# Kernel tuning notes

Measured on AMD Instinct MI355X. Metric: run time of the kernel, lower is better.

Reference implementation:

```python
import jax, jax.numpy as jnp
import numpy as np

DIM = 128
NH = 4
K = 7
PAD = K // 2  # dilation = 1
MLP_HID = 4 * DIM
EPS = 1e-5


def _layernorm(x, w, b):
    m = jnp.mean(x, axis=-1, keepdims=True)
    v = jnp.mean((x - m) ** 2, axis=-1, keepdims=True)
    return (x - m) / jnp.sqrt(v + EPS) * w + b


def _windows(xp, H, W):
    # xp: [B, nh, Hp, Wp, hd] zero-padded; returns [B, nh, H, W, hd, K*K]
    return jnp.stack(
        [xp[:, :, i:i + H, j:j + W, :] for i in range(K) for j in range(K)],
        axis=-1,
    )


def setup_inputs() -> dict:
    key = jax.random.key(0)
    ks = jax.random.split(key, 10)
    s = 0.02
    inp = {
        "x": jax.random.normal(ks[0], (4, 56, 56, DIM), dtype=jnp.float32),
        "ln1_w": jnp.ones((DIM,), jnp.float32),
        "ln1_b": jnp.zeros((DIM,), jnp.float32),
        "w_qkv": jax.random.normal(ks[1], (DIM, 3 * DIM), jnp.float32) * s,
        "b_qkv": jnp.zeros((3 * DIM,), jnp.float32),
        "rpb": jax.random.normal(ks[2], (NH, K * K), jnp.float32) * s,
        "w_proj": jax.random.normal(ks[3], (DIM, DIM), jnp.float32) * s,
        "b_proj": jnp.zeros((DIM,), jnp.float32),
        "ln2_w": jnp.ones((DIM,), jnp.float32),
        "ln2_b": jnp.zeros((DIM,), jnp.float32),
        "w_fc1": jax.random.normal(ks[4], (DIM, MLP_HID), jnp.float32) * s,
        "b_fc1": jnp.zeros((MLP_HID,), jnp.float32),
        "w_fc2": jax.random.normal(ks[5], (MLP_HID, DIM), jnp.float32) * s,
        "b_fc2": jnp.zeros((DIM,), jnp.float32),
    }
    return inp


def _nat_block(x, ln1_w, ln1_b, w_qkv, b_qkv, rpb, w_proj, b_proj,
               ln2_w, ln2_b, w_fc1, b_fc1, w_fc2, b_fc2):
    B, H, W, C = x.shape
    hd = C // NH
    scale = hd ** -0.5

    # --- neighborhood attention ---
    xn = _layernorm(x, ln1_w, ln1_b)
    qkv = xn @ w_qkv + b_qkv                       # [B,H,W,3C]
    qkv = qkv.reshape(B, H, W, 3, NH, hd)
    qkv = jnp.transpose(qkv, (3, 0, 4, 1, 2, 5))   # [3,B,nh,H,W,hd]
    q, k, v = qkv[0] * scale, qkv[1], qkv[2]
    # zero-pad spatial dims (matches F.pad with constant 0 in original)
    pad = ((0, 0), (0, 0), (PAD, PAD), (PAD, PAD), (0, 0))
    kp = jnp.pad(k, pad)
    vp = jnp.pad(v, pad)
    kw = _windows(kp, H, W)                        # [B,nh,H,W,hd,49]
    vw = _windows(vp, H, W)
    attn = jnp.einsum('bnhwd,bnhwdk->bnhwk', q, kw)
    attn = attn + rpb[None, :, None, None, :]
    attn = jax.nn.softmax(attn, axis=-1)
    out = jnp.einsum('bnhwk,bnhwdk->bnhwd', attn, vw)  # [B,nh,H,W,hd]
    out = jnp.transpose(out, (0, 2, 3, 1, 4)).reshape(B, H, W, C)
    x = x + (out @ w_proj + b_proj)

    # --- MLP ---
    xn2 = _layernorm(x, ln2_w, ln2_b)
    h = jax.nn.gelu(xn2 @ w_fc1 + b_fc1, approximate=False)
    x = x + (h @ w_fc2 + b_fc2)
    return x


def reference(x, ln1_w, ln1_b, w_qkv, b_qkv, rpb, w_proj, b_proj,
              ln2_w, ln2_b, w_fc1, b_fc1, w_fc2, b_fc2):
    return _nat_block(x, ln1_w, ln1_b, w_qkv, b_qkv, rpb, w_proj, b_proj,
                      ln2_w, ln2_b, w_fc1, b_fc1, w_fc2, b_fc2)
```

## Files before the change

kernel.cpp:

```cpp
#include <hip/hip_runtime.h>

using bf16x8 = __attribute__((ext_vector_type(8))) short;
using f32x4  = __attribute__((ext_vector_type(4))) float;
typedef unsigned short u16;
typedef __attribute__((ext_vector_type(8))) unsigned short u16x8;
typedef __attribute__((ext_vector_type(4))) unsigned short u16x4;

__device__ __forceinline__ u16 f2b(float f){
  unsigned int i=__float_as_uint(f);
  return (u16)((i + 0x7FFFu + ((i>>16)&1u))>>16);
}
__device__ __forceinline__ float b2f(u16 u){
  union{unsigned int i; float f;}v; v.i=((unsigned int)u)<<16; return v.f;
}
__device__ __forceinline__ void async16(const void* g, void* l){
  __builtin_amdgcn_global_load_lds((__attribute__((address_space(1))) void*)(g),
                                   (__attribute__((address_space(3))) void*)(l), 16, 0, 0);
}
__device__ __forceinline__ float gelu_tanh(float v){
  float u = v*(0.7978845608f + 0.0356774081f*v*v);
  float e = __expf(-2.0f*fabsf(u));
  float th = (1.0f-e)/(1.0f+e);
  th = (u<0.f)? -th : th;
  return 0.5f*v*(1.0f+th);
}

__global__ void prep_kernel(const float* __restrict__ wqkv, const float* __restrict__ wproj,
                            const float* __restrict__ wfc1, const float* __restrict__ wfc2,
                            u16* __restrict__ tqkv, u16* __restrict__ tproj,
                            u16* __restrict__ tfc1, u16* __restrict__ tfc2)
{
  int idx = blockIdx.x*256 + threadIdx.x;
  if (idx < 49152){
    int nc = idx>>14, r = idx&16383, i = r>>3, e = r&7, n = i&127, c = i>>7;
    tqkv[idx] = f2b(wqkv[(c*8+e)*384 + nc*128 + n]);
  } else if (idx < 65536){
    int r = idx-49152; int i=r>>3, e=r&7, n=i&127, c=i>>7;
    tproj[r] = f2b(wproj[(c*8+e)*128 + n]);
  } else if (idx < 131072){
    int t = idx-65536; int nc=t>>14, r=t&16383, i=r>>3, e=r&7, n=i&127, c=i>>7;
    tfc1[t] = f2b(wfc1[(c*8+e)*512 + nc*128 + n]);
  } else if (idx < 196608){
    int t = idx-131072; int nc=t>>14, r=t&16383, i=r>>3, e=r&7, n=i&127, c=i>>7;
    tfc2[t] = f2b(wfc2[(nc*128 + c*8 + e)*128 + n]);
  }
}


__global__ __launch_bounds__(256)
void qkv_ln_kernel(const float* __restrict__ x,
                   const float* __restrict__ ln1w, const float* __restrict__ ln1b,
                   const u16* __restrict__ tqkv, const float* __restrict__ bqkv,
                   u16* __restrict__ qb, u16* __restrict__ kb, u16* __restrict__ vb)
{
  __shared__ __align__(16) char smem[40960];
  char* lA = smem;
  char* lB = smem + 8192;

  const int tid = threadIdx.x;
  const int lane = tid&63, wid = tid>>6;
  const int quad = lane>>4, lrow = lane&15;
  const int m0 = blockIdx.x*32;
  const int nc = blockIdx.y;
  const int wm = (wid&1)*16, wn = (wid>>1)*64;

  #pragma unroll
  for (int kk=0;kk<8;kk++){
    int i = tid + kk*256;
    async16(tqkv + (size_t)nc*16384 + i*8, lB + i*16);
  }

  {
    const int row = tid>>3, g = tid&7;
    float xv[16];
    const float4* xr = (const float4*)(x + (size_t)(m0+row)*128 + g*16);
    float s=0.f, sq=0.f;
    #pragma unroll
    for (int c4=0;c4<4;c4++){
      float4 t = xr[c4];
      xv[c4*4]=t.x; xv[c4*4+1]=t.y; xv[c4*4+2]=t.z; xv[c4*4+3]=t.w;
      s += t.x+t.y+t.z+t.w;
      sq += t.x*t.x+t.y*t.y+t.z*t.z+t.w*t.w;
    }
    s  += __shfl_xor(s,1);  s  += __shfl_xor(s,2);  s  += __shfl_xor(s,4);
    sq += __shfl_xor(sq,1); sq += __shfl_xor(sq,2); sq += __shfl_xor(sq,4);
    float mean = s*0.0078125f;
    float rstd = rsqrtf(sq*0.0078125f - mean*mean + 1e-5f);
    const float4* wr = (const float4*)(ln1w + g*16);
    const float4* br = (const float4*)(ln1b + g*16);
    u16 nv[16];
    #pragma unroll
    for (int c4=0;c4<4;c4++){
      float4 w4 = wr[c4], b4 = br[c4];
      nv[c4*4]   = f2b((xv[c4*4]  -mean)*rstd*w4.x + b4.x);
      nv[c4*4+1] = f2b((xv[c4*4+1]-mean)*rstd*w4.y + b4.y);
      nv[c4*4+2] = f2b((xv[c4*4+2]-mean)*rstd*w4.z + b4.z);
      nv[c4*4+3] = f2b((xv[c4*4+3]-mean)*rstd*w4.w + b4.w);
    }
    #pragma unroll
    for (int cc=0;cc<2;cc++){
      u16x8 pk;
      #pragma unroll
      for (int e=0;e<8;e++) pk[e] = nv[cc*8+e];
      *(u16x8*)(lA + (((g*2+cc)*32 + row)<<4)) = pk;
    }
  }
  __syncthreads();

  f32x4 acc[4] = {};
  #pragma unroll
  for (int ks=0;ks<4;ks++){
    bf16x8 af = ((const bf16x8*)lA)[(ks*4+quad)*32 + wm + lrow];
    #pragma unroll
    for (int j=0;j<4;j++){
      bf16x8 bfr = ((const bf16x8*)lB)[(ks*4+quad)*128 + wn + j*16 + lrow];
      acc[j] = __builtin_amdgcn_mfma_f32_16x16x32_bf16(af, bfr, acc[j], 0,0,0);
    }
  }

  const float scale = 0.17677669529663687f;
  u16* dst = (nc==0)? qb : ((nc==1)? kb : vb);
  #pragma unroll
  for (int j=0;j<4;j++){
    int col = wn + j*16 + lrow;
    float bia = bqkv[nc*128 + col];
    #pragma unroll
    for (int r=0;r<4;r++){
      int row = m0 + wm + quad*4 + r;
      float val = acc[j][r] + bia;
      if (nc==0) val *= scale;
      dst[(size_t)row*128 + col] = f2b(val);
    }
  }
}

#define KT_S 40
#define VT_S 232
#define P_S  152
__global__ __launch_bounds__(256)
void attn_kernel(const u16* __restrict__ qb, const u16* __restrict__ kb,
                 const u16* __restrict__ vb, const float* __restrict__ rpb,
                 u16* __restrict__ aout)
{
  __shared__ __align__(16) char smem[50192];
  u16*  kt   = (u16*)smem;
  u16*  vt   = (u16*)(smem + 15680);
  u16*  Pm   = (u16*)(smem + 30528);
  float* srpb= (float*)(smem + 49984);

  const int tid = threadIdx.x;
  const int tile = blockIdx.x, bh = blockIdx.y;
  const int b = bh>>2, h = bh&3;
  const int ty = (tile/7)*8, tx = (tile%7)*8;
  const int lane = tid&63, wid = tid>>6;
  const int quad = lane>>4, lrow = lane&15;

  #pragma unroll
  for (int kk=0;kk<4;kk++){
    int i = tid + kk*256;
    if (i < 784){
      int pos = i>>2, oct = i&3;
      int hy = pos/14, hx = pos - hy*14;
      int gy = ty + hy - 3, gx = tx + hx - 3;
      u16x8 kv = {0,0,0,0,0,0,0,0};
      if (gy>=0 && gy<56 && gx>=0 && gx<56)
        kv = *(const u16x8*)(kb + ((size_t)(b*3136 + gy*56 + gx)*128 + h*32 + oct*8));
      *(u16x8*)(kt + pos*KT_S + oct*8) = kv;
    }
  }
  #pragma unroll
  for (int kk=0;kk<4;kk++){
    int i = tid + kk*256;
    if (i < 896){
      int pos = i>>2, oct = i&3;
      u16x8 vv = {0,0,0,0,0,0,0,0};
      if (pos < 196){
        int hy = pos/14, hx = pos - hy*14;
        int gy = ty + hy - 3, gx = tx + hx - 3;
        if (gy>=0 && gy<56 && gx>=0 && gx<56)
          vv = *(const u16x8*)(vb + ((size_t)(b*3136 + gy*56 + gx)*128 + h*32 + oct*8));
      }
      #pragma unroll
      for (int j=0;j<8;j++) vt[(oct*8+j)*VT_S + pos] = vv[j];
    }
  }
  if (tid < 49) srpb[tid] = rpb[h*49 + tid];
  __syncthreads();

  const int pxq = wid*16 + lrow;
  const int tokq = b*3136 + (ty + (pxq>>3))*56 + tx + (pxq&7);
  bf16x8 qf = *(const bf16x8*)(qb + (size_t)tokq*128 + h*32 + quad*8);

  f32x4 sc[7];
  const f32x4 zf = {0.f,0.f,0.f,0.f};
  #pragma unroll
  for (int cg=0;cg<7;cg++){
    int pos = wid*28 + cg*16 + lrow;
    bf16x8 kf = *(const bf16x8*)(kt + pos*KT_S + quad*8);
    sc[cg] = __builtin_amdgcn_mfma_f32_16x16x32_bf16(qf, kf, zf, 0,0,0);
  }

  const int lyq = quad>>1;
  #pragma unroll
  for (int cg=0;cg<7;cg++){
    int np = cg*16 + lrow;
    int nh = np/14, hx = np - nh*14;
    int dy = nh - lyq;
    #pragma unroll
    for (int r=0;r<4;r++){
      int lx = (quad*4+r)&7;
      int dx = hx - lx;
      bool in = ((unsigned)dy<7u) && ((unsigned)dx<7u);
      float bias = srpb[in ? (dy*7+dx) : 0];
      sc[cg][r] = in ? (sc[cg][r] + bias) : -1e30f;
    }
  }
  float inv[4];
  #pragma unroll
  for (int r=0;r<4;r++){
    float m = sc[0][r];
    #pragma unroll
    for (int cg=1;cg<7;cg++) m = fmaxf(m, sc[cg][r]);
    m = fmaxf(m, __shfl_xor(m,1)); m = fmaxf(m, __shfl_xor(m,2));
    m = fmaxf(m, __shfl_xor(m,4)); m = fmaxf(m, __shfl_xor(m,8));
    float l = 0.f;
    #pragma unroll
    for (int cg=0;cg<7;cg++){ float p = __expf(sc[cg][r]-m); sc[cg][r]=p; l+=p; }
    l += __shfl_xor(l,1); l += __shfl_xor(l,2);
    l += __shfl_xor(l,4); l += __shfl_xor(l,8);
    inv[r]=1.f/l;
  }

  u16* Pw = Pm + wid*16*P_S;
  #pragma unroll
  for (int cg=0;cg<7;cg++){
    int np = cg*16 + lrow;
    #pragma unroll
    for (int r=0;r<4;r++)
      Pw[(quad*4+r)*P_S + np] = f2b(sc[cg][r]);
  }
  { int zr = lane>>2, seg = lane&3;
    u16x4 z4 = {0,0,0,0};
    *(u16x4*)(Pw + zr*P_S + 112 + seg*4) = z4; }
  __syncthreads();

  f32x4 oacc[2] = {zf, zf};
  #pragma unroll
  for (int ks=0;ks<4;ks++){
    bf16x8 pf = *(const bf16x8*)(Pw + lrow*P_S + ks*32 + quad*8);
    #pragma unroll
    for (int cg2=0;cg2<2;cg2++){
      bf16x8 vf = *(const bf16x8*)(vt + (cg2*16+lrow)*VT_S + wid*28 + ks*32 + quad*8);
      oacc[cg2] = __builtin_amdgcn_mfma_f32_16x16x32_bf16(pf, vf, oacc[cg2], 0,0,0);
    }
  }
  #pragma unroll
  for (int r=0;r<4;r++){
    int px = wid*16 + quad*4 + r;
    int tok = b*3136 + (ty + (px>>3))*56 + tx + (px&7);
    #pragma unroll
    for (int cg2=0;cg2<2;cg2++){
      int ch = h*32 + cg2*16 + lrow;
      aout[(size_t)((tok>>5)*16 + (ch>>3))*256 + (tok&31)*8 + (ch&7)]
        = f2b(oacc[cg2][r]*inv[r]);
    }
  }
}

__global__ __launch_bounds__(256)
void mega_mlp_kernel(const u16* __restrict__ aout, const float* __restrict__ x,
                     const u16* __restrict__ tproj, const float* __restrict__ bproj,
                     const float* __restrict__ ln2w, const float* __restrict__ ln2b,
                     const u16* __restrict__ tfc1, const float* __restrict__ bfc1,
                     const u16* __restrict__ tfc2, const float* __restrict__ bfc2,
                     float* __restrict__ out)
{
  __shared__ __align__(16) char smem[49664];
  char* lA  = smem;
  char* lB  = smem + 8192;
  char* xn2 = smem + 40960;
  float* redS = (float*)(smem + 49152);
  float* redQ = redS + 64;

  const int tid = threadIdx.x;
  const int lane = tid&63, wid = tid>>6;
  const int quad = lane>>4, lrow = lane&15;
  const int m0 = blockIdx.x*32;
  const int wm = (wid&1)*16, wn = (wid>>1)*64;
  const int half = wid>>1;

  #pragma unroll
  for (int kk=0;kk<2;kk++){
    int i = tid + kk*256;
    async16(aout + (size_t)blockIdx.x*4096 + i*8, lA + i*16);
  }
  #pragma unroll
  for (int kk=0;kk<8;kk++){
    int i = tid + kk*256;
    async16(tproj + (size_t)i*8, lB + i*16);
  }
  __syncthreads();

  f32x4 acc[4] = {};
  #pragma unroll
  for (int ks=0;ks<4;ks++){
    bf16x8 af = ((const bf16x8*)lA)[(ks*4+quad)*32 + wm + lrow];
    #pragma unroll
    for (int j=0;j<4;j++){
      bf16x8 bfr = ((const bf16x8*)lB)[(ks*4+quad)*128 + wn + j*16 + lrow];
      acc[j] = __builtin_amdgcn_mfma_f32_16x16x32_bf16(af, bfr, acc[j], 0,0,0);
    }
  }

  float x1v[4][4];
  float ps[4] = {}, pq[4] = {};
  #pragma unroll
  for (int j=0;j<4;j++){
    int col = wn + j*16 + lrow;
    float bia = bproj[col];
    #pragma unroll
    for (int r=0;r<4;r++){
      int row = m0 + wm + quad*4 + r;
      float val = acc[j][r] + bia + x[(size_t)row*128 + col];
      x1v[j][r] = val;
      ps[r] += val; pq[r] += val*val;
    }
  }
  #pragma unroll
  for (int r=0;r<4;r++){
    #pragma unroll
    for (int off=1; off<16; off<<=1){
      ps[r] += __shfl_xor(ps[r], off);
      pq[r] += __shfl_xor(pq[r], off);
    }
  }
  if (lrow==0){
    #pragma unroll
    for (int r=0;r<4;r++){
      int row = wm + quad*4 + r;
      redS[half*32 + row] = ps[r];
      redQ[half*32 + row] = pq[r];
    }
  }
  __syncthreads();

  {
    float w2[4], b2[4];
    #pragma unroll
    for (int j=0;j<4;j++){ int col = wn+j*16+lrow; w2[j]=ln2w[col]; b2[j]=ln2b[col]; }
    #pragma unroll
    for (int r=0;r<4;r++){
      int row = wm + quad*4 + r;
      float mean = (redS[row] + redS[32+row])*0.0078125f;
      float var  = (redQ[row] + redQ[32+row])*0.0078125f - mean*mean;
      float rstd = rsqrtf(var + 1e-5f);
      #pragma unroll
      for (int j=0;j<4;j++){
        int col = wn + j*16 + lrow;
        u16 hv = f2b((x1v[j][r]-mean)*rstd*w2[j] + b2[j]);
        ((u16*)xn2)[((col>>3)*32 + row)*8 + (col&7)] = hv;
      }
    }
  }
  __syncthreads();

  f32x4 acc3[4] = {};
  for (int nc=0; nc<4; nc++){
    if (nc>0) __syncthreads();
    #pragma unroll
    for (int kk=0;kk<8;kk++){
      int i = tid + kk*256;
      async16(tfc1 + (size_t)nc*16384 + i*8, lB + i*16);
    }
    __syncthreads();

    f32x4 acc2[4] = {};
    #pragma unroll
    for (int ks=0;ks<4;ks++){
      bf16x8 af = ((const bf16x8*)xn2)[(ks*4+quad)*32 + wm + lrow];
      #pragma unroll
      for (int j=0;j<4;j++){
        bf16x8 bfr = ((const bf16x8*)lB)[(ks*4+quad)*128 + wn + j*16 + lrow];
        acc2[j] = __builtin_amdgcn_mfma_f32_16x16x32_bf16(af, bfr, acc2[j], 0,0,0);
      }
    }
    #pragma unroll
    for (int j=0;j<4;j++){
      int col = wn + j*16 + lrow;
      float bia = bfc1[nc*128 + col];
      #pragma unroll
      for (int r=0;r<4;r++){
        int row = wm + quad*4 + r;
        float g = gelu_tanh(acc2[j][r] + bia);
        ((u16*)lA)[((col>>3)*32 + row)*8 + (col&7)] = f2b(g);
      }
    }
    __syncthreads();
    #pragma unroll
    for (int kk=0;kk<8;kk++){
      int i = tid + kk*256;
      async16(tfc2 + (size_t)nc*16384 + i*8, lB + i*16);
    }
    __syncthreads();

    #pragma unroll
    for (int ks=0;ks<4;ks++){
      bf16x8 af = ((const bf16x8*)lA)[(ks*4+quad)*32 + wm + lrow];
      #pragma unroll
      for (int j=0;j<4;j++){
        bf16x8 bfr = ((const bf16x8*)lB)[(ks*4+quad)*128 + wn + j*16 + lrow];
        acc3[j] = __builtin_amdgcn_mfma_f32_16x16x32_bf16(af, bfr, acc3[j], 0,0,0);
      }
    }
  }

  #pragma unroll
  for (int j=0;j<4;j++){
    int col = wn + j*16 + lrow;
    float bia = bfc2[col];
    #pragma unroll
    for (int r=0;r<4;r++){
      int row = m0 + wm + quad*4 + r;
      out[(size_t)row*128 + col] = acc3[j][r] + bia + x1v[j][r];
    }
  }
}

extern "C" void kernel_launch(void* const* d_in, const int* in_sizes, int n_in,
                              void* d_out, int out_size, void* d_ws, size_t ws_size,
                              hipStream_t stream)
{
  const float* x     =(const float*)d_in[0];
  const float* ln1w  =(const float*)d_in[1];
  const float* ln1b  =(const float*)d_in[2];
  const float* wqkv  =(const float*)d_in[3];
  const float* bqkv  =(const float*)d_in[4];
  const float* rpb   =(const float*)d_in[5];
  const float* wproj =(const float*)d_in[6];
  const float* bproj =(const float*)d_in[7];
  const float* ln2w  =(const float*)d_in[8];
  const float* ln2b  =(const float*)d_in[9];
  const float* wfc1  =(const float*)d_in[10];
  const float* bfc1  =(const float*)d_in[11];
  const float* wfc2  =(const float*)d_in[12];
  const float* bfc2  =(const float*)d_in[13];

  char* ws=(char*)d_ws;
  size_t o=0;
  u16* tqkv =(u16*)(ws+o); o+=98304;
  u16* tproj=(u16*)(ws+o); o+=32768;
  u16* tfc1 =(u16*)(ws+o); o+=131072;
  u16* tfc2 =(u16*)(ws+o); o+=131072;
  u16* aout =(u16*)(ws+o); o+=3211264;
  u16* qb   =(u16*)(ws+o); o+=3211264;
  u16* kb   =(u16*)(ws+o); o+=3211264;
  u16* vb   =(u16*)(ws+o); o+=3211264;

  prep_kernel<<<768,256,0,stream>>>(wqkv,wproj,wfc1,wfc2,tqkv,tproj,tfc1,tfc2);
  qkv_ln_kernel<<<dim3(392,3),256,0,stream>>>(x,ln1w,ln1b,tqkv,bqkv,qb,kb,vb);
  attn_kernel<<<dim3(49,16),256,0,stream>>>(qb,kb,vb,rpb,aout);
  mega_mlp_kernel<<<392,256,0,stream>>>(aout,x,tproj,bproj,ln2w,ln2b,
                                        tfc1,bfc1,tfc2,bfc2,(float*)d_out);
}
```

Before: 130.0 us.

## Store V channel-major in zero-padded grid and pad K halo rows to 16

The QKV kernel now writes V transposed into a zero-padded per-(batch,head,channel) 64x64 spatial grid, zeroed by the prep kernel. The attention kernel can then load V into LDS with straight vector copies, with no scalar transpose scatter and no bounds checks. The K halo is laid out with 16-wide rows so score tiles line up with halo rows, which simplifies the mask math and removes a barrier and the P zero-fill. In exchange, V writes in the QKV kernel become strided scatters, the zero-fill adds extra memory traffic, and each wave issues one extra MFMA.

Result: slower. 133.3 us (+2.6%).

```diff
diff --git a/kernel.cpp b/kernel.cpp
--- a/kernel.cpp
+++ b/kernel.cpp
@@ -4,7 +4,6 @@
 using f32x4  = __attribute__((ext_vector_type(4))) float;
 typedef unsigned short u16;
 typedef __attribute__((ext_vector_type(8))) unsigned short u16x8;
-typedef __attribute__((ext_vector_type(4))) unsigned short u16x4;
 
 __device__ __forceinline__ u16 f2b(float f){
   unsigned int i=__float_as_uint(f);
@@ -28,7 +27,8 @@
 __global__ void prep_kernel(const float* __restrict__ wqkv, const float* __restrict__ wproj,
                             const float* __restrict__ wfc1, const float* __restrict__ wfc2,
                             u16* __restrict__ tqkv, u16* __restrict__ tproj,
-                            u16* __restrict__ tfc1, u16* __restrict__ tfc2)
+                            u16* __restrict__ tfc1, u16* __restrict__ tfc2,
+                            u16* __restrict__ vb3)
 {
   int idx = blockIdx.x*256 + threadIdx.x;
   if (idx < 49152){
@@ -43,6 +43,10 @@
   } else if (idx < 196608){
     int t = idx-131072; int nc=t>>14, r=t&16383, i=r>>3, e=r&7, n=i&127, c=i>>7;
     tfc2[t] = f2b(wfc2[(nc*128 + c*8 + e)*128 + n]);
+  } else {
+    int zi = idx - 196608;
+    u16x8 z = {0,0,0,0,0,0,0,0};
+    ((u16x8*)vb3)[zi] = z;
   }
 }
 
@@ -51,7 +55,7 @@
 void qkv_ln_kernel(const float* __restrict__ x,
                    const float* __restrict__ ln1w, const float* __restrict__ ln1b,
                    const u16* __restrict__ tqkv, const float* __restrict__ bqkv,
-                   u16* __restrict__ qb, u16* __restrict__ kb, u16* __restrict__ vb)
+                   u16* __restrict__ qb, u16* __restrict__ kb, u16* __restrict__ vb3)
 {
   __shared__ __align__(16) char smem[40960];
   char* lA = smem;
@@ -119,7 +123,6 @@
   }
 
   const float scale = 0.17677669529663687f;
-  u16* dst = (nc==0)? qb : ((nc==1)? kb : vb);
   #pragma unroll
   for (int j=0;j<4;j++){
     int col = wn + j*16 + lrow;
@@ -128,8 +131,16 @@
     for (int r=0;r<4;r++){
       int row = m0 + wm + quad*4 + r;
       float val = acc[j][r] + bia;
-      if (nc==0) val *= scale;
-      dst[(size_t)row*128 + col] = f2b(val);
+      if (nc==0){
+        qb[(size_t)row*128 + col] = f2b(val*scale);
+      } else if (nc==1){
+        kb[(size_t)row*128 + col] = f2b(val);
+      } else {
+        int hh = col>>5, ch = col&31;
+        int bq = row/3136, rem = row - bq*3136;
+        int yy = rem/56, xx = rem - yy*56;
+        vb3[(size_t)(((bq*4+hh)*32 + ch)<<12) + (yy+3)*64 + (xx+3)] = f2b(val);
+      }
     }
   }
 }
@@ -139,14 +150,14 @@
 #define P_S  152
 __global__ __launch_bounds__(256)
 void attn_kernel(const u16* __restrict__ qb, const u16* __restrict__ kb,
-                 const u16* __restrict__ vb, const float* __restrict__ rpb,
+                 const u16* __restrict__ vb3, const float* __restrict__ rpb,
                  u16* __restrict__ aout)
 {
-  __shared__ __align__(16) char smem[50192];
+  __shared__ __align__(16) char smem[52424];
   u16*  kt   = (u16*)smem;
-  u16*  vt   = (u16*)(smem + 15680);
-  u16*  Pm   = (u16*)(smem + 30528);
-  float* srpb= (float*)(smem + 49984);
+  u16*  vt   = (u16*)(smem + 17920);
+  u16*  Pm   = (u16*)(smem + 32768);
+  float* srpb= (float*)(smem + 52224);
 
   const int tid = threadIdx.x;
   const int tile = blockIdx.x, bh = blockIdx.y;
@@ -158,30 +169,26 @@
   #pragma unroll
   for (int kk=0;kk<4;kk++){
     int i = tid + kk*256;
-    if (i < 784){
-      int pos = i>>2, oct = i&3;
-      int hy = pos/14, hx = pos - hy*14;
-      int gy = ty + hy - 3, gx = tx + hx - 3;
-      u16x8 kv = {0,0,0,0,0,0,0,0};
-      if (gy>=0 && gy<56 && gx>=0 && gx<56)
-        kv = *(const u16x8*)(kb + ((size_t)(b*3136 + gy*56 + gx)*128 + h*32 + oct*8));
-      *(u16x8*)(kt + pos*KT_S + oct*8) = kv;
+    if (i < 896){
+      int pos16 = i>>2, oct = i&3;
+      int hx = pos16&15, hy = pos16>>4;
+      if (hx < 14){
+        int gy = ty+hy-3, gx = tx+hx-3;
+        u16x8 kv = {0,0,0,0,0,0,0,0};
+        if ((unsigned)gy<56u && (unsigned)gx<56u)
+          kv = *(const u16x8*)(kb + ((size_t)(b*3136 + gy*56 + gx)*128 + h*32 + oct*8));
+        *(u16x8*)(kt + pos16*KT_S + oct*8) = kv;
+      }
     }
   }
   #pragma unroll
   for (int kk=0;kk<4;kk++){
     int i = tid + kk*256;
     if (i < 896){
-      int pos = i>>2, oct = i&3;
-      u16x8 vv = {0,0,0,0,0,0,0,0};
-      if (pos < 196){
-        int hy = pos/14, hx = pos - hy*14;
-        int gy = ty + hy - 3, gx = tx + hx - 3;
-        if (gy>=0 && gy<56 && gx>=0 && gx<56)
-          vv = *(const u16x8*)(vb + ((size_t)(b*3136 + gy*56 + gx)*128 + h*32 + oct*8));
-      }
-      #pragma unroll
-      for (int j=0;j<8;j++) vt[(oct*8+j)*VT_S + pos] = vv[j];
+      int lo = i&1, t2 = i>>1;
+      int ch = t2/14, hy = t2 - ch*14;
+      *(u16x8*)(vt + ch*VT_S + hy*16 + lo*8) =
+        *(const u16x8*)(vb3 + ((size_t)(bh*32 + ch)<<12) + (ty+hy)*64 + tx + lo*8);
     }
   }
   if (tid < 49) srpb[tid] = rpb[h*49 + tid];
@@ -191,26 +198,24 @@
   const int tokq = b*3136 + (ty + (pxq>>3))*56 + tx + (pxq&7);
   bf16x8 qf = *(const bf16x8*)(qb + (size_t)tokq*128 + h*32 + quad*8);
 
-  f32x4 sc[7];
+  f32x4 sc[8];
   const f32x4 zf = {0.f,0.f,0.f,0.f};
   #pragma unroll
-  for (int cg=0;cg<7;cg++){
-    int pos = wid*28 + cg*16 + lrow;
-    bf16x8 kf = *(const bf16x8*)(kt + pos*KT_S + quad*8);
+  for (int cg=0;cg<8;cg++){
+    bf16x8 kf = *(const bf16x8*)(kt + (wid*32 + cg*16 + lrow)*KT_S + quad*8);
     sc[cg] = __builtin_amdgcn_mfma_f32_16x16x32_bf16(qf, kf, zf, 0,0,0);
   }
 
   const int lyq = quad>>1;
   #pragma unroll
-  for (int cg=0;cg<7;cg++){
-    int np = cg*16 + lrow;
-    int nh = np/14, hx = np - nh*14;
-    int dy = nh - lyq;
+  for (int cg=0;cg<8;cg++){
+    int dy = cg - lyq;
+    bool rowok = ((unsigned)dy < 7u) && (lrow < 14);
     #pragma unroll
     for (int r=0;r<4;r++){
       int lx = (quad*4+r)&7;
-      int dx = hx - lx;
-      bool in = ((unsigned)dy<7u) && ((unsigned)dx<7u);
+      int dx = lrow - lx;
+      bool in = rowok && ((unsigned)dx < 7u);
       float bias = srpb[in ? (dy*7+dx) : 0];
       sc[cg][r] = in ? (sc[cg][r] + bias) : -1e30f;
     }
@@ -220,12 +225,12 @@
   for (int r=0;r<4;r++){
     float m = sc[0][r];
     #pragma unroll
-    for (int cg=1;cg<7;cg++) m = fmaxf(m, sc[cg][r]);
+    for (int cg=1;cg<8;cg++) m = fmaxf(m, sc[cg][r]);
     m = fmaxf(m, __shfl_xor(m,1)); m = fmaxf(m, __shfl_xor(m,2));
     m = fmaxf(m, __shfl_xor(m,4)); m = fmaxf(m, __shfl_xor(m,8));
     float l = 0.f;
     #pragma unroll
-    for (int cg=0;cg<7;cg++){ float p = __expf(sc[cg][r]-m); sc[cg][r]=p; l+=p; }
+    for (int cg=0;cg<8;cg++){ float p = __expf(sc[cg][r]-m); sc[cg][r]=p; l+=p; }
     l += __shfl_xor(l,1); l += __shfl_xor(l,2);
     l += __shfl_xor(l,4); l += __shfl_xor(l,8);
     inv[r]=1.f/l;
@@ -233,16 +238,11 @@
 
   u16* Pw = Pm + wid*16*P_S;
   #pragma unroll
-  for (int cg=0;cg<7;cg++){
-    int np = cg*16 + lrow;
+  for (int cg=0;cg<8;cg++){
     #pragma unroll
     for (int r=0;r<4;r++)
-      Pw[(quad*4+r)*P_S + np] = f2b(sc[cg][r]);
-  }
-  { int zr = lane>>2, seg = lane&3;
-    u16x4 z4 = {0,0,0,0};
-    *(u16x4*)(Pw + zr*P_S + 112 + seg*4) = z4; }
-  __syncthreads();
+      Pw[(quad*4+r)*P_S + cg*16 + lrow] = f2b(sc[cg][r]);
+  }
 
   f32x4 oacc[2] = {zf, zf};
   #pragma unroll
@@ -250,7 +250,7 @@
     bf16x8 pf = *(const bf16x8*)(Pw + lrow*P_S + ks*32 + quad*8);
     #pragma unroll
     for (int cg2=0;cg2<2;cg2++){
-      bf16x8 vf = *(const bf16x8*)(vt + (cg2*16+lrow)*VT_S + wid*28 + ks*32 + quad*8);
+      bf16x8 vf = *(const bf16x8*)(vt + (cg2*16+lrow)*VT_S + wid*32 + ks*32 + quad*8);
       oacc[cg2] = __builtin_amdgcn_mfma_f32_16x16x32_bf16(pf, vf, oacc[cg2], 0,0,0);
     }
   }
@@ -454,11 +454,11 @@
   u16* aout =(u16*)(ws+o); o+=3211264;
   u16* qb   =(u16*)(ws+o); o+=3211264;
   u16* kb   =(u16*)(ws+o); o+=3211264;
-  u16* vb   =(u16*)(ws+o); o+=3211264;
-
-  prep_kernel<<<768,256,0,stream>>>(wqkv,wproj,wfc1,wfc2,tqkv,tproj,tfc1,tfc2);
-  qkv_ln_kernel<<<dim3(392,3),256,0,stream>>>(x,ln1w,ln1b,tqkv,bqkv,qb,kb,vb);
-  attn_kernel<<<dim3(49,16),256,0,stream>>>(qb,kb,vb,rpb,aout);
+  u16* vb3  =(u16*)(ws+o); o+=4194304;
+
+  prep_kernel<<<1792,256,0,stream>>>(wqkv,wproj,wfc1,wfc2,tqkv,tproj,tfc1,tfc2,vb3);
+  qkv_ln_kernel<<<dim3(392,3),256,0,stream>>>(x,ln1w,ln1b,tqkv,bqkv,qb,kb,vb3);
+  attn_kernel<<<dim3(49,16),256,0,stream>>>(qb,kb,vb3,rpb,aout);
   mega_mlp_kernel<<<392,256,0,stream>>>(aout,x,tproj,bproj,ln2w,ln2b,
                                         tfc1,bfc1,tfc2,bfc2,(float*)d_out);
 }
```
